# Optimization experiments

Measured on AMD Instinct MI355X. Metric: run time of the kernel, lower is better.

The kernel has to match this reference:

```python
import jax, jax.numpy as jnp
import numpy as np

BATCH, DIM, ORDER = 16384, 1024, 3

def setup_inputs() -> dict:
    key = jax.random.key(0)
    k1, k2, k3 = jax.random.split(key, 3)
    x0 = jax.random.normal(k1, (BATCH, DIM), dtype=jnp.float32)
    # xavier-uniform init scale for w of shape (d, 1): sqrt(6/(d+1))
    limit = float(np.sqrt(6.0 / (DIM + 1)))
    W = jax.random.uniform(k2, (ORDER, DIM), dtype=jnp.float32, minval=-limit, maxval=limit)
    B = jnp.zeros((ORDER, DIM), dtype=jnp.float32)
    return {"x0": x0, "W": W, "B": B}

def reference(x0, W, B):
    # CrossLayer: xi_next = (x0 xi^T) w + b + xi == x0 * (xi . w) + b + xi
    # (outer product followed by matmul with w collapses to a dot-product scale)
    xi = x0
    for l in range(W.shape[0]):  # small fixed number of cross layers
        s = xi @ W[l]                      # [B]  dot(xi, w_l)
        xi = x0 * s[:, None] + B[l] + xi   # [B, D]
    return xi
```

## Files before the change

kernel.cpp:

```cpp
#include <hip/hip_runtime.h>


#define CN_BATCH 16384
#define CN_DIM   1024

#define WAVES_PER_BLOCK 4
#define ROWS_PER_WAVE   4
#define ROWS_PER_BLOCK  (WAVES_PER_BLOCK * ROWS_PER_WAVE)

typedef float f32x4 __attribute__((ext_vector_type(4)));

__global__ __launch_bounds__(256, 4) void
crossnet_kernel(const float* __restrict__ x0,
                const float* __restrict__ W,
                const float* __restrict__ B,
                float* __restrict__ out)
{
    const int tid  = threadIdx.x;
    const int wave = tid >> 6;
    const int lane = tid & 63;
    const int off0 = lane * 4;

    f32x4 w0[4], w1[4], w2[4], bs[4];
    float t1 = 0.f, t2 = 0.f;
#pragma unroll
    for (int c = 0; c < 4; ++c) {
        const int off = c * 256 + off0;
        w0[c] = *reinterpret_cast<const f32x4*>(W + 0 * CN_DIM + off);
        w1[c] = *reinterpret_cast<const f32x4*>(W + 1 * CN_DIM + off);
        w2[c] = *reinterpret_cast<const f32x4*>(W + 2 * CN_DIM + off);
        const f32x4 b0 = *reinterpret_cast<const f32x4*>(B + 0 * CN_DIM + off);
        const f32x4 b1 = *reinterpret_cast<const f32x4*>(B + 1 * CN_DIM + off);
        const f32x4 b2 = *reinterpret_cast<const f32x4*>(B + 2 * CN_DIM + off);
        bs[c] = b0 + b1 + b2;
        t1 = fmaf(b0.x, w1[c].x, t1); t1 = fmaf(b0.y, w1[c].y, t1);
        t1 = fmaf(b0.z, w1[c].z, t1); t1 = fmaf(b0.w, w1[c].w, t1);
        t2 = fmaf(b0.x + b1.x, w2[c].x, t2); t2 = fmaf(b0.y + b1.y, w2[c].y, t2);
        t2 = fmaf(b0.z + b1.z, w2[c].z, t2); t2 = fmaf(b0.w + b1.w, w2[c].w, t2);
    }
#pragma unroll
    for (int o = 1; o < 64; o <<= 1) {
        t1 += __shfl_xor(t1, o, 64);
        t2 += __shfl_xor(t2, o, 64);
    }

    const size_t row0 = ((size_t)blockIdx.x * WAVES_PER_BLOCK + wave) * ROWS_PER_WAVE;
    const float* __restrict__ xr = x0 + row0 * (size_t)CN_DIM;

    f32x4 cur[4], nxt[4];
#pragma unroll
    for (int c = 0; c < 4; ++c)
        cur[c] = __builtin_nontemporal_load(
            reinterpret_cast<const f32x4*>(xr + c * 256 + off0));

#pragma unroll
    for (int r = 0; r < ROWS_PER_WAVE; ++r) {
        if (r + 1 < ROWS_PER_WAVE) {
#pragma unroll
            for (int c = 0; c < 4; ++c)
                nxt[c] = __builtin_nontemporal_load(
                    reinterpret_cast<const f32x4*>(
                        xr + (size_t)(r + 1) * CN_DIM + c * 256 + off0));
        }

        float a0 = 0.f, a1 = 0.f, a2 = 0.f;
#pragma unroll
        for (int c = 0; c < 4; ++c) {
            a0 = fmaf(cur[c].x, w0[c].x, a0); a0 = fmaf(cur[c].y, w0[c].y, a0);
            a0 = fmaf(cur[c].z, w0[c].z, a0); a0 = fmaf(cur[c].w, w0[c].w, a0);
            a1 = fmaf(cur[c].x, w1[c].x, a1); a1 = fmaf(cur[c].y, w1[c].y, a1);
            a1 = fmaf(cur[c].z, w1[c].z, a1); a1 = fmaf(cur[c].w, w1[c].w, a1);
            a2 = fmaf(cur[c].x, w2[c].x, a2); a2 = fmaf(cur[c].y, w2[c].y, a2);
            a2 = fmaf(cur[c].z, w2[c].z, a2); a2 = fmaf(cur[c].w, w2[c].w, a2);
        }

#pragma unroll
        for (int o = 1; o < 64; o <<= 1) {
            a0 += __shfl_xor(a0, o, 64);
            a1 += __shfl_xor(a1, o, 64);
            a2 += __shfl_xor(a2, o, 64);
        }

        const float s0 = a0;
        const float s1 = fmaf(1.f + s0, a1, t1);
        const float s2 = fmaf(1.f + s0 + s1, a2, t2);
        const float cf = 1.f + s0 + s1 + s2;

        float* __restrict__ orow = out + (row0 + (size_t)r) * CN_DIM;
#pragma unroll
        for (int c = 0; c < 4; ++c) {
            f32x4 o;
            o.x = fmaf(cur[c].x, cf, bs[c].x);
            o.y = fmaf(cur[c].y, cf, bs[c].y);
            o.z = fmaf(cur[c].z, cf, bs[c].z);
            o.w = fmaf(cur[c].w, cf, bs[c].w);
            __builtin_nontemporal_store(o,
                reinterpret_cast<f32x4*>(orow + c * 256 + off0));
        }

#pragma unroll
        for (int c = 0; c < 4; ++c) cur[c] = nxt[c];
    }
}

extern "C" void kernel_launch(void* const* d_in, const int* in_sizes, int n_in,
                              void* d_out, int out_size, void* d_ws, size_t ws_size,
                              hipStream_t stream)
{
    const float* x0 = (const float*)d_in[0];
    const float* W  = (const float*)d_in[1];
    const float* B  = (const float*)d_in[2];
    float* out      = (float*)d_out;

    dim3 grid(CN_BATCH / ROWS_PER_BLOCK);
    dim3 block(WAVES_PER_BLOCK * 64);
    crossnet_kernel<<<grid, block, 0, stream>>>(x0, W, B, out);
}
```

Before: 125.5 us.

## Precompute bias terms in prologue kernel and batch row loads per wave

Adds a small one-block kernel that folds the summed bias and the two bias-weight dot products into a workspace buffer, so the main kernel reads these instead of recomputing them in every block. The main kernel now handles 2 rows per wave, issues all row loads up front instead of software-pipelining them, and interleaves the per-row dot products so one shuffle reduction pass covers both rows. Weights are re-read per chunk instead of staying in registers, and loads and stores lose their nontemporal hints. The change adds a second kernel launch and doubles the grid size.

```diff
diff --git a/kernel.cpp b/kernel.cpp
--- a/kernel.cpp
+++ b/kernel.cpp
@@ -5,101 +5,145 @@
 #define CN_DIM   1024
 
 #define WAVES_PER_BLOCK 4
-#define ROWS_PER_WAVE   4
+#define ROWS_PER_WAVE   2
 #define ROWS_PER_BLOCK  (WAVES_PER_BLOCK * ROWS_PER_WAVE)
+#define GRID_BLOCKS     (CN_BATCH / ROWS_PER_BLOCK)
 
 typedef float f32x4 __attribute__((ext_vector_type(4)));
 
+__device__ __forceinline__ float fma4(f32x4 x, f32x4 w, float acc) {
+    acc = fmaf(x.x, w.x, acc); acc = fmaf(x.y, w.y, acc);
+    acc = fmaf(x.z, w.z, acc); acc = fmaf(x.w, w.w, acc);
+    return acc;
+}
+
+__global__ __launch_bounds__(256) void
+crossnet_pre(const float* __restrict__ W, const float* __restrict__ B,
+             float* __restrict__ pre)
+{
+    const int t    = threadIdx.x;
+    const int wave = t >> 6;
+    const int lane = t & 63;
+
+    const f32x4 b0 = *reinterpret_cast<const f32x4*>(B + 0 * CN_DIM + t * 4);
+    const f32x4 b1 = *reinterpret_cast<const f32x4*>(B + 1 * CN_DIM + t * 4);
+    const f32x4 b2 = *reinterpret_cast<const f32x4*>(B + 2 * CN_DIM + t * 4);
+    const f32x4 w1 = *reinterpret_cast<const f32x4*>(W + 1 * CN_DIM + t * 4);
+    const f32x4 w2 = *reinterpret_cast<const f32x4*>(W + 2 * CN_DIM + t * 4);
+
+    *reinterpret_cast<f32x4*>(pre + t * 4) = b0 + b1 + b2;
+
+    float p1 = fma4(b0, w1, 0.f);
+    float p2 = fma4(b0 + b1, w2, 0.f);
+#pragma unroll
+    for (int o = 1; o < 64; o <<= 1) {
+        p1 += __shfl_xor(p1, o, 64);
+        p2 += __shfl_xor(p2, o, 64);
+    }
+    __shared__ float sh1[WAVES_PER_BLOCK], sh2[WAVES_PER_BLOCK];
+    if (lane == 0) { sh1[wave] = p1; sh2[wave] = p2; }
+    __syncthreads();
+    if (t == 0) {
+        pre[CN_DIM]     = sh1[0] + sh1[1] + sh1[2] + sh1[3];
+        pre[CN_DIM + 1] = sh2[0] + sh2[1] + sh2[2] + sh2[3];
+    }
+}
+
+template<bool PRE>
 __global__ __launch_bounds__(256, 4) void
-crossnet_kernel(const float* __restrict__ x0,
-                const float* __restrict__ W,
-                const float* __restrict__ B,
-                float* __restrict__ out)
+crossnet_main(const float* __restrict__ x0, const float* __restrict__ W,
+              const float* __restrict__ B,  const float* __restrict__ pre,
+              float* __restrict__ out)
 {
     const int tid  = threadIdx.x;
     const int wave = tid >> 6;
     const int lane = tid & 63;
     const int off0 = lane * 4;
 
-    f32x4 w0[4], w1[4], w2[4], bs[4];
-    float t1 = 0.f, t2 = 0.f;
+    const size_t row0 = ((size_t)blockIdx.x * WAVES_PER_BLOCK + wave) * ROWS_PER_WAVE;
+    const float* __restrict__ xr = x0 + row0 * CN_DIM;
+
+    f32x4 xv[ROWS_PER_WAVE][4];
+#pragma unroll
+    for (int r = 0; r < ROWS_PER_WAVE; ++r)
+#pragma unroll
+        for (int c = 0; c < 4; ++c)
+            xv[r][c] = *reinterpret_cast<const f32x4*>(xr + r * CN_DIM + c * 256 + off0);
+
+    f32x4 bs[4];
+    float t1, t2;
+    if (PRE) {
+#pragma unroll
+        for (int c = 0; c < 4; ++c)
+            bs[c] = *reinterpret_cast<const f32x4*>(pre + c * 256 + off0);
+        t1 = pre[CN_DIM];
+        t2 = pre[CN_DIM + 1];
+    } else {
+        t1 = 0.f; t2 = 0.f;
+#pragma unroll
+        for (int c = 0; c < 4; ++c) {
+            const int off = c * 256 + off0;
+            const f32x4 b0 = *reinterpret_cast<const f32x4*>(B + 0 * CN_DIM + off);
+            const f32x4 b1 = *reinterpret_cast<const f32x4*>(B + 1 * CN_DIM + off);
+            const f32x4 b2 = *reinterpret_cast<const f32x4*>(B + 2 * CN_DIM + off);
+            const f32x4 w1 = *reinterpret_cast<const f32x4*>(W + 1 * CN_DIM + off);
+            const f32x4 w2 = *reinterpret_cast<const f32x4*>(W + 2 * CN_DIM + off);
+            bs[c] = b0 + b1 + b2;
+            t1 = fma4(b0, w1, t1);
+            t2 = fma4(b0 + b1, w2, t2);
+        }
+#pragma unroll
+        for (int o = 1; o < 64; o <<= 1) {
+            t1 += __shfl_xor(t1, o, 64);
+            t2 += __shfl_xor(t2, o, 64);
+        }
+    }
+
+    float a[ROWS_PER_WAVE][3];
+#pragma unroll
+    for (int r = 0; r < ROWS_PER_WAVE; ++r) {
+        a[r][0] = 0.f; a[r][1] = 0.f; a[r][2] = 0.f;
+    }
 #pragma unroll
     for (int c = 0; c < 4; ++c) {
         const int off = c * 256 + off0;
-        w0[c] = *reinterpret_cast<const f32x4*>(W + 0 * CN_DIM + off);
-        w1[c] = *reinterpret_cast<const f32x4*>(W + 1 * CN_DIM + off);
-        w2[c] = *reinterpret_cast<const f32x4*>(W + 2 * CN_DIM + off);
-        const f32x4 b0 = *reinterpret_cast<const f32x4*>(B + 0 * CN_DIM + off);
-        const f32x4 b1 = *reinterpret_cast<const f32x4*>(B + 1 * CN_DIM + off);
-        const f32x4 b2 = *reinterpret_cast<const f32x4*>(B + 2 * CN_DIM + off);
-        bs[c] = b0 + b1 + b2;
-        t1 = fmaf(b0.x, w1[c].x, t1); t1 = fmaf(b0.y, w1[c].y, t1);
-        t1 = fmaf(b0.z, w1[c].z, t1); t1 = fmaf(b0.w, w1[c].w, t1);
-        t2 = fmaf(b0.x + b1.x, w2[c].x, t2); t2 = fmaf(b0.y + b1.y, w2[c].y, t2);
-        t2 = fmaf(b0.z + b1.z, w2[c].z, t2); t2 = fmaf(b0.w + b1.w, w2[c].w, t2);
+        const f32x4 w0 = *reinterpret_cast<const f32x4*>(W + 0 * CN_DIM + off);
+        const f32x4 w1 = *reinterpret_cast<const f32x4*>(W + 1 * CN_DIM + off);
+        const f32x4 w2 = *reinterpret_cast<const f32x4*>(W + 2 * CN_DIM + off);
+#pragma unroll
+        for (int r = 0; r < ROWS_PER_WAVE; ++r) {
+            a[r][0] = fma4(xv[r][c], w0, a[r][0]);
+            a[r][1] = fma4(xv[r][c], w1, a[r][1]);
+            a[r][2] = fma4(xv[r][c], w2, a[r][2]);
+        }
     }
+
 #pragma unroll
     for (int o = 1; o < 64; o <<= 1) {
-        t1 += __shfl_xor(t1, o, 64);
-        t2 += __shfl_xor(t2, o, 64);
+#pragma unroll
+        for (int r = 0; r < ROWS_PER_WAVE; ++r) {
+            a[r][0] += __shfl_xor(a[r][0], o, 64);
+            a[r][1] += __shfl_xor(a[r][1], o, 64);
+            a[r][2] += __shfl_xor(a[r][2], o, 64);
+        }
     }
-
-    const size_t row0 = ((size_t)blockIdx.x * WAVES_PER_BLOCK + wave) * ROWS_PER_WAVE;
-    const float* __restrict__ xr = x0 + row0 * (size_t)CN_DIM;
-
-    f32x4 cur[4], nxt[4];
-#pragma unroll
-    for (int c = 0; c < 4; ++c)
-        cur[c] = __builtin_nontemporal_load(
-            reinterpret_cast<const f32x4*>(xr + c * 256 + off0));
 
 #pragma unroll
     for (int r = 0; r < ROWS_PER_WAVE; ++r) {
-        if (r + 1 < ROWS_PER_WAVE) {
-#pragma unroll
-            for (int c = 0; c < 4; ++c)
-                nxt[c] = __builtin_nontemporal_load(
-                    reinterpret_cast<const f32x4*>(
-                        xr + (size_t)(r + 1) * CN_DIM + c * 256 + off0));
-        }
-
-        float a0 = 0.f, a1 = 0.f, a2 = 0.f;
-#pragma unroll
-        for (int c = 0; c < 4; ++c) {
-            a0 = fmaf(cur[c].x, w0[c].x, a0); a0 = fmaf(cur[c].y, w0[c].y, a0);
-            a0 = fmaf(cur[c].z, w0[c].z, a0); a0 = fmaf(cur[c].w, w0[c].w, a0);
-            a1 = fmaf(cur[c].x, w1[c].x, a1); a1 = fmaf(cur[c].y, w1[c].y, a1);
-            a1 = fmaf(cur[c].z, w1[c].z, a1); a1 = fmaf(cur[c].w, w1[c].w, a1);
-            a2 = fmaf(cur[c].x, w2[c].x, a2); a2 = fmaf(cur[c].y, w2[c].y, a2);
-            a2 = fmaf(cur[c].z, w2[c].z, a2); a2 = fmaf(cur[c].w, w2[c].w, a2);
-        }
-
-#pragma unroll
-        for (int o = 1; o < 64; o <<= 1) {
-            a0 += __shfl_xor(a0, o, 64);
-            a1 += __shfl_xor(a1, o, 64);
-            a2 += __shfl_xor(a2, o, 64);
-        }
-
-        const float s0 = a0;
-        const float s1 = fmaf(1.f + s0, a1, t1);
-        const float s2 = fmaf(1.f + s0 + s1, a2, t2);
+        const float s0 = a[r][0];
+        const float s1 = fmaf(1.f + s0, a[r][1], t1);
+        const float s2 = fmaf(1.f + s0 + s1, a[r][2], t2);
         const float cf = 1.f + s0 + s1 + s2;
-
-        float* __restrict__ orow = out + (row0 + (size_t)r) * CN_DIM;
+        float* __restrict__ orow = out + (row0 + r) * CN_DIM;
 #pragma unroll
         for (int c = 0; c < 4; ++c) {
             f32x4 o;
-            o.x = fmaf(cur[c].x, cf, bs[c].x);
-            o.y = fmaf(cur[c].y, cf, bs[c].y);
-            o.z = fmaf(cur[c].z, cf, bs[c].z);
-            o.w = fmaf(cur[c].w, cf, bs[c].w);
-            __builtin_nontemporal_store(o,
-                reinterpret_cast<f32x4*>(orow + c * 256 + off0));
+            o.x = fmaf(xv[r][c].x, cf, bs[c].x);
+            o.y = fmaf(xv[r][c].y, cf, bs[c].y);
+            o.z = fmaf(xv[r][c].z, cf, bs[c].z);
+            o.w = fmaf(xv[r][c].w, cf, bs[c].w);
+            *reinterpret_cast<f32x4*>(orow + c * 256 + off0) = o;
         }
-
-#pragma unroll
-        for (int c = 0; c < 4; ++c) cur[c] = nxt[c];
     }
 }
 
@@ -112,7 +156,14 @@
     const float* B  = (const float*)d_in[2];
     float* out      = (float*)d_out;
 
-    dim3 grid(CN_BATCH / ROWS_PER_BLOCK);
+    dim3 grid(GRID_BLOCKS);
     dim3 block(WAVES_PER_BLOCK * 64);
-    crossnet_kernel<<<grid, block, 0, stream>>>(x0, W, B, out);
+
+    if (d_ws != nullptr && ws_size >= (size_t)(CN_DIM + 2) * sizeof(float)) {
+        float* pre = (float*)d_ws;
+        crossnet_pre<<<dim3(1), dim3(256), 0, stream>>>(W, B, pre);
+        crossnet_main<true><<<grid, block, 0, stream>>>(x0, W, B, pre, out);
+    } else {
+        crossnet_main<false><<<grid, block, 0, stream>>>(x0, W, B, nullptr, out);
+    }
 }
```

Measured after the change: 118.1 us. 5.9% less time.

## Issue all row loads up front, batch reductions, halve rows per wave

Applied to the files above, without the earlier changes.

Moves the x0 row loads to the start of the kernel, before the W/B parameter loads, so memory latency overlaps the setup work. All rows' dot products are computed and their cross-lane shuffle reductions are interleaved together with the bias-term reductions. Rows per wave drop from 4 to 2, which doubles the grid, and nontemporal loads and stores are replaced with plain ones. This raises per-block W/B setup overhead and may change cache behaviour for the streamed data.

```diff
diff --git a/kernel.cpp b/kernel.cpp
--- a/kernel.cpp
+++ b/kernel.cpp
@@ -5,10 +5,17 @@
 #define CN_DIM   1024
 
 #define WAVES_PER_BLOCK 4
-#define ROWS_PER_WAVE   4
+#define ROWS_PER_WAVE   2
 #define ROWS_PER_BLOCK  (WAVES_PER_BLOCK * ROWS_PER_WAVE)
+#define GRID_BLOCKS     (CN_BATCH / ROWS_PER_BLOCK)
 
 typedef float f32x4 __attribute__((ext_vector_type(4)));
+
+__device__ __forceinline__ float fma4(f32x4 x, f32x4 w, float acc) {
+    acc = fmaf(x.x, w.x, acc); acc = fmaf(x.y, w.y, acc);
+    acc = fmaf(x.z, w.z, acc); acc = fmaf(x.w, w.w, acc);
+    return acc;
+}
 
 __global__ __launch_bounds__(256, 4) void
 crossnet_kernel(const float* __restrict__ x0,
@@ -20,6 +27,16 @@
     const int wave = tid >> 6;
     const int lane = tid & 63;
     const int off0 = lane * 4;
+
+    const size_t row0 = ((size_t)blockIdx.x * WAVES_PER_BLOCK + wave) * ROWS_PER_WAVE;
+    const float* __restrict__ xr = x0 + row0 * CN_DIM;
+
+    f32x4 xv[ROWS_PER_WAVE][4];
+#pragma unroll
+    for (int r = 0; r < ROWS_PER_WAVE; ++r)
+#pragma unroll
+        for (int c = 0; c < 4; ++c)
+            xv[r][c] = *reinterpret_cast<const f32x4*>(xr + r * CN_DIM + c * 256 + off0);
 
     f32x4 w0[4], w1[4], w2[4], bs[4];
     float t1 = 0.f, t2 = 0.f;
@@ -33,73 +50,53 @@
         const f32x4 b1 = *reinterpret_cast<const f32x4*>(B + 1 * CN_DIM + off);
         const f32x4 b2 = *reinterpret_cast<const f32x4*>(B + 2 * CN_DIM + off);
         bs[c] = b0 + b1 + b2;
-        t1 = fmaf(b0.x, w1[c].x, t1); t1 = fmaf(b0.y, w1[c].y, t1);
-        t1 = fmaf(b0.z, w1[c].z, t1); t1 = fmaf(b0.w, w1[c].w, t1);
-        t2 = fmaf(b0.x + b1.x, w2[c].x, t2); t2 = fmaf(b0.y + b1.y, w2[c].y, t2);
-        t2 = fmaf(b0.z + b1.z, w2[c].z, t2); t2 = fmaf(b0.w + b1.w, w2[c].w, t2);
+        t1 = fma4(b0, w1[c], t1);
+        t2 = fma4(b0 + b1, w2[c], t2);
+    }
+
+    float a[ROWS_PER_WAVE][3];
+#pragma unroll
+    for (int r = 0; r < ROWS_PER_WAVE; ++r) {
+        a[r][0] = 0.f; a[r][1] = 0.f; a[r][2] = 0.f;
     }
 #pragma unroll
+    for (int c = 0; c < 4; ++c) {
+#pragma unroll
+        for (int r = 0; r < ROWS_PER_WAVE; ++r) {
+            a[r][0] = fma4(xv[r][c], w0[c], a[r][0]);
+            a[r][1] = fma4(xv[r][c], w1[c], a[r][1]);
+            a[r][2] = fma4(xv[r][c], w2[c], a[r][2]);
+        }
+    }
+
+#pragma unroll
     for (int o = 1; o < 64; o <<= 1) {
+#pragma unroll
+        for (int r = 0; r < ROWS_PER_WAVE; ++r) {
+            a[r][0] += __shfl_xor(a[r][0], o, 64);
+            a[r][1] += __shfl_xor(a[r][1], o, 64);
+            a[r][2] += __shfl_xor(a[r][2], o, 64);
+        }
         t1 += __shfl_xor(t1, o, 64);
         t2 += __shfl_xor(t2, o, 64);
     }
 
-    const size_t row0 = ((size_t)blockIdx.x * WAVES_PER_BLOCK + wave) * ROWS_PER_WAVE;
-    const float* __restrict__ xr = x0 + row0 * (size_t)CN_DIM;
-
-    f32x4 cur[4], nxt[4];
-#pragma unroll
-    for (int c = 0; c < 4; ++c)
-        cur[c] = __builtin_nontemporal_load(
-            reinterpret_cast<const f32x4*>(xr + c * 256 + off0));
-
 #pragma unroll
     for (int r = 0; r < ROWS_PER_WAVE; ++r) {
-        if (r + 1 < ROWS_PER_WAVE) {
-#pragma unroll
-            for (int c = 0; c < 4; ++c)
-                nxt[c] = __builtin_nontemporal_load(
-                    reinterpret_cast<const f32x4*>(
-                        xr + (size_t)(r + 1) * CN_DIM + c * 256 + off0));
-        }
-
-        float a0 = 0.f, a1 = 0.f, a2 = 0.f;
-#pragma unroll
-        for (int c = 0; c < 4; ++c) {
-            a0 = fmaf(cur[c].x, w0[c].x, a0); a0 = fmaf(cur[c].y, w0[c].y, a0);
-            a0 = fmaf(cur[c].z, w0[c].z, a0); a0 = fmaf(cur[c].w, w0[c].w, a0);
-            a1 = fmaf(cur[c].x, w1[c].x, a1); a1 = fmaf(cur[c].y, w1[c].y, a1);
-            a1 = fmaf(cur[c].z, w1[c].z, a1); a1 = fmaf(cur[c].w, w1[c].w, a1);
-            a2 = fmaf(cur[c].x, w2[c].x, a2); a2 = fmaf(cur[c].y, w2[c].y, a2);
-            a2 = fmaf(cur[c].z, w2[c].z, a2); a2 = fmaf(cur[c].w, w2[c].w, a2);
-        }
-
-#pragma unroll
-        for (int o = 1; o < 64; o <<= 1) {
-            a0 += __shfl_xor(a0, o, 64);
-            a1 += __shfl_xor(a1, o, 64);
-            a2 += __shfl_xor(a2, o, 64);
-        }
-
-        const float s0 = a0;
-        const float s1 = fmaf(1.f + s0, a1, t1);
-        const float s2 = fmaf(1.f + s0 + s1, a2, t2);
+        const float s0 = a[r][0];
+        const float s1 = fmaf(1.f + s0, a[r][1], t1);
+        const float s2 = fmaf(1.f + s0 + s1, a[r][2], t2);
         const float cf = 1.f + s0 + s1 + s2;
-
-        float* __restrict__ orow = out + (row0 + (size_t)r) * CN_DIM;
+        float* __restrict__ orow = out + (row0 + r) * CN_DIM;
 #pragma unroll
         for (int c = 0; c < 4; ++c) {
             f32x4 o;
-            o.x = fmaf(cur[c].x, cf, bs[c].x);
-            o.y = fmaf(cur[c].y, cf, bs[c].y);
-            o.z = fmaf(cur[c].z, cf, bs[c].z);
-            o.w = fmaf(cur[c].w, cf, bs[c].w);
-            __builtin_nontemporal_store(o,
-                reinterpret_cast<f32x4*>(orow + c * 256 + off0));
+            o.x = fmaf(xv[r][c].x, cf, bs[c].x);
+            o.y = fmaf(xv[r][c].y, cf, bs[c].y);
+            o.z = fmaf(xv[r][c].z, cf, bs[c].z);
+            o.w = fmaf(xv[r][c].w, cf, bs[c].w);
+            *reinterpret_cast<f32x4*>(orow + c * 256 + off0) = o;
         }
-
-#pragma unroll
-        for (int c = 0; c < 4; ++c) cur[c] = nxt[c];
     }
 }
 
@@ -112,7 +109,7 @@
     const float* B  = (const float*)d_in[2];
     float* out      = (float*)d_out;
 
-    dim3 grid(CN_BATCH / ROWS_PER_BLOCK);
+    dim3 grid(GRID_BLOCKS);
     dim3 block(WAVES_PER_BLOCK * 64);
     crossnet_kernel<<<grid, block, 0, stream>>>(x0, W, B, out);
 }
```

Result: faster. 117.9 us (-6.1%).
